# Kernel tuning notes

Hardware: AMD Instinct MI355X
Metric: run time of the kernel (lower is better)

Reference implementation:

```python
import jax, jax.numpy as jnp
import numpy as np

NUM_NODES = 65536       # B * gcn_nodes_num = 256 * 256
NODES_PER_GRAPH = 256
GCN_EMB_DIM = 128
N_EMBD = 512
NUM_EDGES = 1048576     # avg degree 16
NEG_SLOPE = 0.1


def gcn_conv(x, edge_index, W, b, num_nodes):
    """PyG GCNConv: add self-loops, symmetric normalization, linear, aggregate."""
    loop = jnp.arange(num_nodes, dtype=edge_index.dtype)
    src = jnp.concatenate([edge_index[0], loop])
    dst = jnp.concatenate([edge_index[1], loop])
    deg = jax.ops.segment_sum(jnp.ones_like(dst, dtype=x.dtype), dst,
                              num_segments=num_nodes)
    dinv = jnp.where(deg > 0, jax.lax.rsqrt(deg), jnp.zeros_like(deg))
    norm = dinv[src] * dinv[dst]              # [E+N]
    h = x @ W                                 # [N, out]
    msg = h[src] * norm[:, None]              # [E+N, out]
    out = jax.ops.segment_sum(msg, dst, num_segments=num_nodes)
    return out + b


def setup_inputs() -> dict:
    key = jax.random.key(0)
    ks = jax.random.split(key, 8)
    nodes = jax.random.normal(ks[0], (NUM_NODES, 3), dtype=jnp.float32)
    edge_index = jax.random.randint(ks[1], (2, NUM_EDGES), 0, NUM_NODES,
                                    dtype=jnp.int64)
    W1 = jax.random.normal(ks[2], (3, 3), dtype=jnp.float32) * 0.5
    b1 = jnp.zeros((3,), dtype=jnp.float32)
    W2 = jax.random.normal(ks[3], (3, GCN_EMB_DIM), dtype=jnp.float32) * 0.5
    b2 = jnp.zeros((GCN_EMB_DIM,), dtype=jnp.float32)
    W3 = jax.random.normal(ks[4], (GCN_EMB_DIM * NODES_PER_GRAPH, N_EMBD),
                           dtype=jnp.float32) * 0.01
    b3 = jnp.zeros((N_EMBD,), dtype=jnp.float32)
    return {"nodes": nodes, "edge_index": edge_index,
            "W1": W1, "b1": b1, "W2": W2, "b2": b2, "W3": W3, "b3": b3}


def reference(nodes, edge_index, W1, b1, W2, b2, W3, b3):
    n = nodes.shape[0]
    h = gcn_conv(nodes, edge_index, W1, b1, n)           # GCNConv(3,3)
    h = jnp.where(h >= 0, h, NEG_SLOPE * h)              # leaky_relu(0.1)
    h = gcn_conv(h, edge_index, W2, b2, n)               # GCNConv(3,128)
    h = h.reshape(-1, GCN_EMB_DIM * NODES_PER_GRAPH)     # [B, 128*256]
    out = h @ W3 + b3                                    # [B, 512]
    return out
```

## Files before the change

### kernel.cpp

```cpp
#include <hip/hip_runtime.h>

static constexpr int NN   = 65536;
static constexpr int NPG  = 256;
static constexpr int NB   = 256;
static constexpr int EMB  = 128;
static constexpr int NOUT = 512;

static constexpr int NBIN = 256;
static constexpr int CAP  = 4608;

static constexpr int BT = 8;
static constexpr int KS = 16;
static constexpr int IC = NPG / KS;

__global__ __launch_bounds__(1024)
void k_partV(const int* __restrict__ src, const int* __restrict__ dst, int E,
             int* __restrict__ gbin, int* __restrict__ part,
             const float* __restrict__ W2, const float* __restrict__ b2,
             const float* __restrict__ W3, float4* __restrict__ V4) {
    union SH {
        struct { int hist[NBIN]; int loff[NBIN]; int base[NBIN]; int scanbuf[NBIN];
                 int stage[4096]; } part;
        struct { float red[2][4][NOUT]; } bv;
    };
    __shared__ SH sh;
    int tid = threadIdx.x;
    int bid = blockIdx.x;

    if (bid >= NBIN) {
        int i = bid - NBIN;
        int j = tid & 511;
        int half = tid >> 9;
        const float* w3 = W3 + (size_t)i * EMB * NOUT + (size_t)half * 64 * NOUT + j;
        float a0 = 0.f, a1 = 0.f, a2 = 0.f, a3 = 0.f;
        for (int c = 0; c < 64; c++) {
            float v = w3[(size_t)c * NOUT];
            int cc = half * 64 + c;
            a0 += W2[0*EMB+cc] * v;
            a1 += W2[1*EMB+cc] * v;
            a2 += W2[2*EMB+cc] * v;
            a3 += b2[cc]       * v;
        }
        sh.bv.red[half][0][j] = a0;
        sh.bv.red[half][1][j] = a1;
        sh.bv.red[half][2][j] = a2;
        sh.bv.red[half][3][j] = a3;
        __syncthreads();
        if (tid < NOUT) {
            float4 r;
            r.x = sh.bv.red[0][0][tid] + sh.bv.red[1][0][tid];
            r.y = sh.bv.red[0][1][tid] + sh.bv.red[1][1][tid];
            r.z = sh.bv.red[0][2][tid] + sh.bv.red[1][2][tid];
            r.w = sh.bv.red[0][3][tid] + sh.bv.red[1][3][tid];
            V4[(size_t)i * NOUT + tid] = r;
        }
        return;
    }
    int epb = (E + NBIN - 1) / NBIN;
    int e0 = bid * epb;
    int e1 = min(e0 + epb, E);
    if (tid < NBIN) sh.part.hist[tid] = 0;
    __syncthreads();

    int pk[4], bn[4], rk[4];
    int n = 0;
    int e = e0 + tid * 4;
    if (e + 4 <= e1) {
        int4 s4 = *(const int4*)(src + e);
        int4 d4 = *(const int4*)(dst + e);
        int ss[4] = {s4.x, s4.y, s4.z, s4.w};
        int dd[4] = {d4.x, d4.y, d4.z, d4.w};
#pragma unroll
        for (int k = 0; k < 4; k++) {
            pk[k] = ss[k] | ((dd[k] & 255) << 16);
            bn[k] = dd[k] >> 8;
            rk[k] = atomicAdd(&sh.part.hist[bn[k]], 1);
        }
        n = 4;
    } else {
        for (int k = 0; k < 4 && e + k < e1; k++) {
            int s = src[e+k], d = dst[e+k];
            pk[n] = s | ((d & 255) << 16);
            bn[n] = d >> 8;
            rk[n] = atomicAdd(&sh.part.hist[bn[n]], 1);
            n++;
        }
    }
    __syncthreads();

    if (tid < NBIN) sh.part.scanbuf[tid] = sh.part.hist[tid];
    __syncthreads();
    for (int off = 1; off < NBIN; off <<= 1) {
        int v = 0;
        if (tid < NBIN && tid >= off) v = sh.part.scanbuf[tid - off];
        __syncthreads();
        if (tid < NBIN) sh.part.scanbuf[tid] += v;
        __syncthreads();
    }
    if (tid < NBIN) {
        sh.part.loff[tid] = sh.part.scanbuf[tid] - sh.part.hist[tid];
        sh.part.base[tid] = atomicAdd(&gbin[tid], sh.part.hist[tid]);
    }
    __syncthreads();

    for (int k = 0; k < n; k++) sh.part.stage[sh.part.loff[bn[k]] + rk[k]] = pk[k];
    __syncthreads();

    int bin = tid >> 2;
    int cnt = sh.part.hist[bin], bs = sh.part.base[bin], lo = sh.part.loff[bin];
    for (int t = tid & 3; t < cnt; t += 4) {
        int gp = bs + t;
        if (gp < CAP) part[bin * CAP + gp] = sh.part.stage[lo + t];
    }
}

__global__ __launch_bounds__(512)
void k_csr(const int* __restrict__ gbin, const int* __restrict__ part,
           const float* __restrict__ nodes,
           float* __restrict__ dinv, float4* __restrict__ y1,
           int* __restrict__ rs, unsigned short* __restrict__ srt) {
    __shared__ int pkst[CAP];
    __shared__ int hist[NPG], scanb[NPG], off_[NPG];
    __shared__ unsigned short stageS[CAP];
    int tid = threadIdx.x, bin = blockIdx.x;
    if (tid < NPG) hist[tid] = 0;
    __syncthreads();
    int cnt = min(gbin[bin], CAP);
    const int* pp = part + (size_t)bin * CAP;
    for (int e = tid; e < cnt; e += 512) {
        int p = pp[e];
        pkst[e] = p;
        atomicAdd(&hist[(p >> 16) & 255], 1);
    }
    __syncthreads();
    if (tid < NPG) scanb[tid] = hist[tid];
    __syncthreads();
    for (int off = 1; off < NPG; off <<= 1) {
        int v = 0;
        if (tid < NPG && tid >= off) v = scanb[tid - off];
        __syncthreads();
        if (tid < NPG) scanb[tid] += v;
        __syncthreads();
    }
    if (tid < NPG) {
        int start = scanb[tid] - hist[tid];
        off_[tid] = start;
        int node = bin * NPG + tid;
        float di = rsqrtf((float)(hist[tid] + 1));
        dinv[node] = di;
        y1[node] = make_float4(nodes[3*node+0] * di, nodes[3*node+1] * di,
                               nodes[3*node+2] * di, 0.f);
        rs[node] = start | (hist[tid] << 20);
    }
    __syncthreads();
    for (int e = tid; e < cnt; e += 512) {
        int p = pkst[e];
        int pos = atomicAdd(&off_[(p >> 16) & 255], 1);
        stageS[pos] = (unsigned short)(p & 0xFFFF);
    }
    __syncthreads();
    const unsigned int* so = (const unsigned int*)stageS;
    unsigned int* g = (unsigned int*)(srt + (size_t)bin * CAP);
    for (int t = tid; t < (cnt + 1) >> 1; t += 512) g[t] = so[t];
}

__device__ __forceinline__ void agg_pass(int g, const int* __restrict__ rs,
                                         const unsigned short* __restrict__ srt,
                                         const float* __restrict__ dinv,
                                         const float* __restrict__ W1,
                                         const float* __restrict__ b1,
                                         const float4* __restrict__ yin,
                                         float4* __restrict__ yout, bool first) {
    int i = g >> 3, sub = g & 7;
    int rsd = rs[i];
    int start = rsd & 0xFFFFF, deg = rsd >> 20;
    const unsigned short* sp = srt + (size_t)(i >> 8) * CAP + start;
    float ax = 0.f, ay = 0.f, az = 0.f;
    for (int k = sub; k < deg; k += 8) {
        float4 v = yin[sp[k]];
        ax += v.x; ay += v.y; az += v.z;
    }
    ax += __shfl_xor(ax, 1); ay += __shfl_xor(ay, 1); az += __shfl_xor(az, 1);
    ax += __shfl_xor(ax, 2); ay += __shfl_xor(ay, 2); az += __shfl_xor(az, 2);
    ax += __shfl_xor(ax, 4); ay += __shfl_xor(ay, 4); az += __shfl_xor(az, 4);
    if (sub == 0) {
        float4 self = yin[i];
        float di = dinv[i];
        float a0 = (ax + self.x) * di, a1 = (ay + self.y) * di, a2 = (az + self.z) * di;
        if (first) {
            float h[3];
#pragma unroll
            for (int k = 0; k < 3; k++) {
                float t = a0 * W1[0*3+k] + a1 * W1[1*3+k] + a2 * W1[2*3+k] + b1[k];
                t = (t >= 0.f) ? t : 0.1f * t;
                h[k] = t * di;
            }
            yout[i] = make_float4(h[0], h[1], h[2], 0.f);
        } else {
            yout[i] = make_float4(a0, a1, a2, 0.f);
        }
    }
}

__global__ void k_agg1(const int* __restrict__ rs, const unsigned short* __restrict__ srt,
                       const float* __restrict__ dinv, const float4* __restrict__ y1,
                       const float* __restrict__ W1, const float* __restrict__ b1,
                       float4* __restrict__ y2) {
    agg_pass(blockIdx.x * 256 + threadIdx.x, rs, srt, dinv, W1, b1, y1, y2, true);
}

__global__ void k_agg2(const int* __restrict__ rs, const unsigned short* __restrict__ srt,
                       const float* __restrict__ dinv, const float4* __restrict__ y2,
                       float4* __restrict__ agg2) {
    agg_pass(blockIdx.x * 256 + threadIdx.x, rs, srt, dinv, nullptr, nullptr,
             y2, agg2, false);
}

__global__ void k_out_part(const float4* __restrict__ agg2, const float4* __restrict__ V4,
                           float* __restrict__ part) {
    __shared__ float4 a_s[BT * IC];
    int tid = threadIdx.x;
    int j  = blockIdx.x * 256 + tid;
    int b0 = blockIdx.y * BT;
    int i0 = blockIdx.z * IC;
    for (int idx = tid; idx < BT * IC; idx += 256) {
        int t = idx / IC, i = idx % IC;
        a_s[idx] = agg2[(size_t)(b0 + t) * NPG + i0 + i];
    }
    __syncthreads();

    float acc[BT];
#pragma unroll
    for (int t = 0; t < BT; t++) acc[t] = 0.f;

    const float4* vj = V4 + (size_t)i0 * NOUT + j;
    for (int i = 0; i < IC; i++) {
        float4 v = vj[(size_t)i * NOUT];
#pragma unroll
        for (int t = 0; t < BT; t++) {
            float4 a = a_s[t*IC + i];
            acc[t] += a.x * v.x + a.y * v.y + a.z * v.z + v.w;
        }
    }
#pragma unroll
    for (int t = 0; t < BT; t++)
        part[((size_t)blockIdx.z * NB + b0 + t) * NOUT + j] = acc[t];
}

__global__ void k_reduce(const float4* __restrict__ part4, const float4* __restrict__ b3_4,
                         float4* __restrict__ out4) {
    int idx = blockIdx.x * 256 + threadIdx.x;
    int j4 = idx & (NOUT/4 - 1);
    float4 acc = b3_4[j4];
#pragma unroll
    for (int s = 0; s < KS; s++) {
        float4 v = part4[(size_t)s * (NB*NOUT/4) + idx];
        acc.x += v.x; acc.y += v.y; acc.z += v.z; acc.w += v.w;
    }
    out4[idx] = acc;
}

extern "C" void kernel_launch(void* const* d_in, const int* in_sizes, int n_in,
                              void* d_out, int out_size, void* d_ws, size_t ws_size,
                              hipStream_t stream) {
    const float* nodes = (const float*)d_in[0];
    const int*   ei    = (const int*)  d_in[1];
    const float* W1    = (const float*)d_in[2];
    const float* b1    = (const float*)d_in[3];
    const float* W2    = (const float*)d_in[4];
    const float* b2    = (const float*)d_in[5];
    const float* W3    = (const float*)d_in[6];
    const float* b3    = (const float*)d_in[7];

    const int E = in_sizes[1] / 2;
    const int* src = ei;
    const int* dst = ei + E;

    char* ws = (char*)d_ws;
    int*    gbin  = (int*)ws;
    float4* y1    = (float4*)(ws + 1024);
    float4* y2    = y1 + NN;
    float4* agg2  = y2 + NN;
    float4* V4    = agg2 + NN;
    float*  partO = (float*)(V4 + (size_t)NPG * NOUT);
    int*    partE = (int*)(partO + (size_t)KS * NB * NOUT);
    unsigned short* srt = (unsigned short*)(partE + (size_t)NBIN * CAP);
    int*    rs    = (int*)(srt + (size_t)NBIN * CAP);
    float*  dinv  = (float*)(rs + NN);

    hipMemsetAsync(gbin, 0, NBIN * 4, stream);
    k_partV   <<<2*NBIN, 1024, 0, stream>>>(src, dst, E, gbin, partE, W2, b2, W3, V4);
    k_csr     <<<NBIN,    512, 0, stream>>>(gbin, partE, nodes, dinv, y1, rs, srt);
    k_agg1    <<<NN*8/256, 256, 0, stream>>>(rs, srt, dinv, y1, W1, b1, y2);
    k_agg2    <<<NN*8/256, 256, 0, stream>>>(rs, srt, dinv, y2, agg2);
    k_out_part<<<dim3(2, NB/BT, KS), 256, 0, stream>>>(agg2, V4, partO);
    k_reduce  <<<NB*NOUT/4/256,      256, 0, stream>>>((const float4*)partO,
                                                       (const float4*)b3, (float4*)d_out);
}
```

Baseline: 168.2 us.

## Replace global bin atomics with per-block slots, fuse split-K reduce via last-block

Edge partitioning now writes each block's per-bin edges into fixed per-(bin,block) slots with a count array instead of using global atomic offsets, which removes the memset and the global atomics. The CSR kernel scans those slots directly with 1024 threads rather than staging a contiguous list. The final split-K reduction is fused into the output kernel: the last block to arrive for each tile does the reduction, with the tile counters cleared in k_agg2, so one launch goes away. The W2·W3 precompute is also vectorized to float4 with an 8-way channel split. Slots are capped at 44 edges per bin per block, so a denser bin would silently drop edges, and the CSR pass now walks padded slots.

```diff
diff --git a/kernel.cpp b/kernel.cpp
--- a/kernel.cpp
+++ b/kernel.cpp
@@ -6,53 +6,69 @@
 static constexpr int EMB  = 128;
 static constexpr int NOUT = 512;
 
-static constexpr int NBIN = 256;
-static constexpr int CAP  = 4608;
+static constexpr int NBIN  = 256;
+static constexpr int SLOTB = 44;
+static constexpr int NSLOT = NBIN * SLOTB;
+static constexpr int CAP   = 4608;
 
 static constexpr int BT = 8;
 static constexpr int KS = 16;
 static constexpr int IC = NPG / KS;
 
-__global__ __launch_bounds__(1024)
+__global__ __launch_bounds__(1024, 2)
 void k_partV(const int* __restrict__ src, const int* __restrict__ dst, int E,
-             int* __restrict__ gbin, int* __restrict__ part,
+             int* __restrict__ cntA, int* __restrict__ partE,
              const float* __restrict__ W2, const float* __restrict__ b2,
              const float* __restrict__ W3, float4* __restrict__ V4) {
     union SH {
-        struct { int hist[NBIN]; int loff[NBIN]; int base[NBIN]; int scanbuf[NBIN];
+        struct { int hist[NBIN]; int loff[NBIN]; int scanbuf[NBIN];
                  int stage[4096]; } part;
-        struct { float red[2][4][NOUT]; } bv;
+        struct { float4 red[8][4][128]; } bv;
     };
     __shared__ SH sh;
     int tid = threadIdx.x;
     int bid = blockIdx.x;
 
     if (bid >= NBIN) {
-        int i = bid - NBIN;
-        int j = tid & 511;
-        int half = tid >> 9;
-        const float* w3 = W3 + (size_t)i * EMB * NOUT + (size_t)half * 64 * NOUT + j;
-        float a0 = 0.f, a1 = 0.f, a2 = 0.f, a3 = 0.f;
-        for (int c = 0; c < 64; c++) {
-            float v = w3[(size_t)c * NOUT];
-            int cc = half * 64 + c;
-            a0 += W2[0*EMB+cc] * v;
-            a1 += W2[1*EMB+cc] * v;
-            a2 += W2[2*EMB+cc] * v;
-            a3 += b2[cc]       * v;
-        }
-        sh.bv.red[half][0][j] = a0;
-        sh.bv.red[half][1][j] = a1;
-        sh.bv.red[half][2][j] = a2;
-        sh.bv.red[half][3][j] = a3;
+        int i  = bid - NBIN;
+        int j4 = tid & 127;
+        int cg = tid >> 7;
+        const float4* w3 = (const float4*)(W3 + (size_t)i * EMB * NOUT)
+                           + (size_t)cg * 16 * (NOUT/4) + j4;
+        float4 a0 = {0,0,0,0}, a1 = {0,0,0,0}, a2 = {0,0,0,0}, a3 = {0,0,0,0};
+        for (int c = 0; c < 16; c++) {
+            float4 v = w3[(size_t)c * (NOUT/4)];
+            int cc = cg*16 + c;
+            float w0 = W2[0*EMB+cc], w1 = W2[1*EMB+cc], w2 = W2[2*EMB+cc], wb = b2[cc];
+            a0.x += w0*v.x; a0.y += w0*v.y; a0.z += w0*v.z; a0.w += w0*v.w;
+            a1.x += w1*v.x; a1.y += w1*v.y; a1.z += w1*v.z; a1.w += w1*v.w;
+            a2.x += w2*v.x; a2.y += w2*v.y; a2.z += w2*v.z; a2.w += w2*v.w;
+            a3.x += wb*v.x; a3.y += wb*v.y; a3.z += wb*v.z; a3.w += wb*v.w;
+        }
+        sh.bv.red[cg][0][j4] = a0;
+        sh.bv.red[cg][1][j4] = a1;
+        sh.bv.red[cg][2][j4] = a2;
+        sh.bv.red[cg][3][j4] = a3;
+        __syncthreads();
+        if (tid < 512) {
+            int k = tid >> 7, jj = tid & 127;
+            float4 s = sh.bv.red[0][k][jj];
+#pragma unroll
+            for (int g = 1; g < 8; g++) {
+                float4 v = sh.bv.red[g][k][jj];
+                s.x += v.x; s.y += v.y; s.z += v.z; s.w += v.w;
+            }
+            sh.bv.red[0][k][jj] = s;
+        }
         __syncthreads();
         if (tid < NOUT) {
-            float4 r;
-            r.x = sh.bv.red[0][0][tid] + sh.bv.red[1][0][tid];
-            r.y = sh.bv.red[0][1][tid] + sh.bv.red[1][1][tid];
-            r.z = sh.bv.red[0][2][tid] + sh.bv.red[1][2][tid];
-            r.w = sh.bv.red[0][3][tid] + sh.bv.red[1][3][tid];
-            V4[(size_t)i * NOUT + tid] = r;
+            int j = tid;
+            const float* r0 = (const float*)&sh.bv.red[0][0][j >> 2];
+            const float* r1 = (const float*)&sh.bv.red[0][1][j >> 2];
+            const float* r2 = (const float*)&sh.bv.red[0][2][j >> 2];
+            const float* r3 = (const float*)&sh.bv.red[0][3][j >> 2];
+            float4 o = { r0[j & 3], r1[j & 3], r2[j & 3], r3[j & 3] };
+            V4[(size_t)i * NOUT + j] = o;
         }
         return;
     }
@@ -97,40 +113,38 @@
         if (tid < NBIN) sh.part.scanbuf[tid] += v;
         __syncthreads();
     }
-    if (tid < NBIN) {
-        sh.part.loff[tid] = sh.part.scanbuf[tid] - sh.part.hist[tid];
-        sh.part.base[tid] = atomicAdd(&gbin[tid], sh.part.hist[tid]);
-    }
+    if (tid < NBIN) sh.part.loff[tid] = sh.part.scanbuf[tid] - sh.part.hist[tid];
     __syncthreads();
 
     for (int k = 0; k < n; k++) sh.part.stage[sh.part.loff[bn[k]] + rk[k]] = pk[k];
     __syncthreads();
 
     int bin = tid >> 2;
-    int cnt = sh.part.hist[bin], bs = sh.part.base[bin], lo = sh.part.loff[bin];
-    for (int t = tid & 3; t < cnt; t += 4) {
-        int gp = bs + t;
-        if (gp < CAP) part[bin * CAP + gp] = sh.part.stage[lo + t];
-    }
-}
-
-__global__ __launch_bounds__(512)
-void k_csr(const int* __restrict__ gbin, const int* __restrict__ part,
+    int cnt = min(sh.part.hist[bin], SLOTB);
+    int lo  = sh.part.loff[bin];
+    int gb  = bin * NSLOT + bid * SLOTB;
+    for (int t = tid & 3; t < cnt; t += 4) partE[gb + t] = sh.part.stage[lo + t];
+    if ((tid & 3) == 0) cntA[bin * NBIN + bid] = cnt;
+}
+
+__global__ __launch_bounds__(1024)
+void k_csr(const int* __restrict__ cntA, const int* __restrict__ partE,
            const float* __restrict__ nodes,
            float* __restrict__ dinv, float4* __restrict__ y1,
            int* __restrict__ rs, unsigned short* __restrict__ srt) {
-    __shared__ int pkst[CAP];
+    __shared__ int cnts[NBIN];
     __shared__ int hist[NPG], scanb[NPG], off_[NPG];
     __shared__ unsigned short stageS[CAP];
     int tid = threadIdx.x, bin = blockIdx.x;
     if (tid < NPG) hist[tid] = 0;
-    __syncthreads();
-    int cnt = min(gbin[bin], CAP);
-    const int* pp = part + (size_t)bin * CAP;
-    for (int e = tid; e < cnt; e += 512) {
-        int p = pp[e];
-        pkst[e] = p;
-        atomicAdd(&hist[(p >> 16) & 255], 1);
+    if (tid < NBIN) cnts[tid] = cntA[bin * NBIN + tid];
+    __syncthreads();
+
+    const int* pp = partE + (size_t)bin * NSLOT;
+    for (int t = tid; t < NSLOT; t += 1024) {
+        int blk = t / SLOTB, slot = t - blk * SLOTB;
+        if (slot < cnts[blk])
+            atomicAdd(&hist[(pp[t] >> 16) & 255], 1);
     }
     __syncthreads();
     if (tid < NPG) scanb[tid] = hist[tid];
@@ -153,15 +167,19 @@
         rs[node] = start | (hist[tid] << 20);
     }
     __syncthreads();
-    for (int e = tid; e < cnt; e += 512) {
-        int p = pkst[e];
-        int pos = atomicAdd(&off_[(p >> 16) & 255], 1);
-        stageS[pos] = (unsigned short)(p & 0xFFFF);
-    }
-    __syncthreads();
+    for (int t = tid; t < NSLOT; t += 1024) {
+        int blk = t / SLOTB, slot = t - blk * SLOTB;
+        if (slot < cnts[blk]) {
+            int p = pp[t];
+            int pos = atomicAdd(&off_[(p >> 16) & 255], 1);
+            stageS[pos] = (unsigned short)(p & 0xFFFF);
+        }
+    }
+    __syncthreads();
+    int tot = scanb[NPG - 1];
     const unsigned int* so = (const unsigned int*)stageS;
     unsigned int* g = (unsigned int*)(srt + (size_t)bin * CAP);
-    for (int t = tid; t < (cnt + 1) >> 1; t += 512) g[t] = so[t];
+    for (int t = tid; t < (tot + 1) >> 1; t += 1024) g[t] = so[t];
 }
 
 __device__ __forceinline__ void agg_pass(int g, const int* __restrict__ rs,
@@ -211,14 +229,18 @@
 
 __global__ void k_agg2(const int* __restrict__ rs, const unsigned short* __restrict__ srt,
                        const float* __restrict__ dinv, const float4* __restrict__ y2,
-                       float4* __restrict__ agg2) {
+                       float4* __restrict__ agg2, int* __restrict__ tc) {
+    if (blockIdx.x == 0 && threadIdx.x < 64) tc[threadIdx.x] = 0;
     agg_pass(blockIdx.x * 256 + threadIdx.x, rs, srt, dinv, nullptr, nullptr,
              y2, agg2, false);
 }
 
-__global__ void k_out_part(const float4* __restrict__ agg2, const float4* __restrict__ V4,
-                           float* __restrict__ part) {
+__global__ __launch_bounds__(256)
+void k_out(const float4* __restrict__ agg2, const float4* __restrict__ V4,
+           const float* __restrict__ b3, float* __restrict__ partO,
+           int* __restrict__ tc, float* __restrict__ out) {
     __shared__ float4 a_s[BT * IC];
+    __shared__ int lastFlag;
     int tid = threadIdx.x;
     int j  = blockIdx.x * 256 + tid;
     int b0 = blockIdx.y * BT;
@@ -244,20 +266,24 @@
     }
 #pragma unroll
     for (int t = 0; t < BT; t++)
-        part[((size_t)blockIdx.z * NB + b0 + t) * NOUT + j] = acc[t];
-}
-
-__global__ void k_reduce(const float4* __restrict__ part4, const float4* __restrict__ b3_4,
-                         float4* __restrict__ out4) {
-    int idx = blockIdx.x * 256 + threadIdx.x;
-    int j4 = idx & (NOUT/4 - 1);
-    float4 acc = b3_4[j4];
-#pragma unroll
-    for (int s = 0; s < KS; s++) {
-        float4 v = part4[(size_t)s * (NB*NOUT/4) + idx];
-        acc.x += v.x; acc.y += v.y; acc.z += v.z; acc.w += v.w;
-    }
-    out4[idx] = acc;
+        partO[((size_t)blockIdx.z * NB + b0 + t) * NOUT + j] = acc[t];
+
+    __threadfence();
+    __syncthreads();
+    int tile = blockIdx.y * 2 + blockIdx.x;
+    if (tid == 0) lastFlag = (atomicAdd(&tc[tile], 1) == KS - 1);
+    __syncthreads();
+    if (!lastFlag) return;
+
+    __threadfence();
+    float bj = b3[j];
+    for (int t = 0; t < BT; t++) {
+        float r = bj;
+#pragma unroll
+        for (int s = 0; s < KS; s++)
+            r += partO[((size_t)s * NB + b0 + t) * NOUT + j];
+        out[(size_t)(b0 + t) * NOUT + j] = r;
+    }
 }
 
 extern "C" void kernel_launch(void* const* d_in, const int* in_sizes, int n_in,
@@ -277,23 +303,21 @@
     const int* dst = ei + E;
 
     char* ws = (char*)d_ws;
-    int*    gbin  = (int*)ws;
-    float4* y1    = (float4*)(ws + 1024);
+    float4* y1    = (float4*)ws;
     float4* y2    = y1 + NN;
     float4* agg2  = y2 + NN;
     float4* V4    = agg2 + NN;
     float*  partO = (float*)(V4 + (size_t)NPG * NOUT);
     int*    partE = (int*)(partO + (size_t)KS * NB * NOUT);
-    unsigned short* srt = (unsigned short*)(partE + (size_t)NBIN * CAP);
+    unsigned short* srt = (unsigned short*)(partE + (size_t)NBIN * NSLOT);
     int*    rs    = (int*)(srt + (size_t)NBIN * CAP);
     float*  dinv  = (float*)(rs + NN);
-
-    hipMemsetAsync(gbin, 0, NBIN * 4, stream);
-    k_partV   <<<2*NBIN, 1024, 0, stream>>>(src, dst, E, gbin, partE, W2, b2, W3, V4);
-    k_csr     <<<NBIN,    512, 0, stream>>>(gbin, partE, nodes, dinv, y1, rs, srt);
-    k_agg1    <<<NN*8/256, 256, 0, stream>>>(rs, srt, dinv, y1, W1, b1, y2);
-    k_agg2    <<<NN*8/256, 256, 0, stream>>>(rs, srt, dinv, y2, agg2);
-    k_out_part<<<dim3(2, NB/BT, KS), 256, 0, stream>>>(agg2, V4, partO);
-    k_reduce  <<<NB*NOUT/4/256,      256, 0, stream>>>((const float4*)partO,
-                                                       (const float4*)b3, (float4*)d_out);
-}
+    int*    cntA  = (int*)(dinv + NN);
+    int*    tc    = cntA + NBIN * NBIN;
+
+    k_partV<<<2*NBIN, 1024, 0, stream>>>(src, dst, E, cntA, partE, W2, b2, W3, V4);
+    k_csr  <<<NBIN,   1024, 0, stream>>>(cntA, partE, nodes, dinv, y1, rs, srt);
+    k_agg1 <<<NN*8/256, 256, 0, stream>>>(rs, srt, dinv, y1, W1, b1, y2);
+    k_agg2 <<<NN*8/256, 256, 0, stream>>>(rs, srt, dinv, y2, agg2, tc);
+    k_out  <<<dim3(2, NB/BT, KS), 256, 0, stream>>>(agg2, V4, b3, partO, tc, (float*)d_out);
+}
```

Result: slower. 257.6 us (+53.1%).
